# Kernel optimization log

Hardware: AMD Instinct MI355X
Metric: run time of the kernel (lower is better)

The kernel has to match this reference:

```python
import jax, jax.numpy as jnp
import numpy as np

NL = 4      # num_layers
DM = 1024   # hidden_size (d_model)
DI = 2048   # d_inner = expand * d_model
DS = 16     # d_state
DC = 4      # d_conv
DTR = 64    # dt_rank = ceil(d_model/16)
IN = 256    # input_size
OUT = 128   # output_size
B = 4096    # batch


def setup_inputs() -> dict:
    key = jax.random.key(0)
    ks = jax.random.split(key, 10)
    s = 0.02
    d = {}
    d['x'] = jax.random.normal(ks[0], (B, IN), dtype=jnp.float32)
    d['inp_w'] = jax.random.normal(ks[1], (DM, IN), dtype=jnp.float32) * s
    d['inp_b'] = jnp.zeros((DM,), jnp.float32)
    d['in_proj_w'] = jax.random.normal(ks[2], (NL, 2 * DI, DM), dtype=jnp.float32) * s
    d['conv_w'] = jax.random.normal(ks[3], (NL, DI, DC), dtype=jnp.float32) * s
    d['conv_b'] = jnp.zeros((NL, DI), jnp.float32)
    d['xproj_w'] = jax.random.normal(ks[4], (NL, DTR + 2 * DS, DI), dtype=jnp.float32) * s
    d['dt_w'] = jax.random.normal(ks[5], (NL, DI, DTR), dtype=jnp.float32) * s
    dt_init = jax.random.uniform(ks[6], (NL, DI), minval=1e-3, maxval=1e-1)
    d['dt_b'] = jnp.log(jnp.expm1(dt_init))  # softplus^-1 of target dt
    d['A_log'] = jnp.log(jnp.broadcast_to(jnp.arange(1, DS + 1, dtype=jnp.float32), (NL, DI, DS)))
    d['D_param'] = jnp.ones((NL, DI), jnp.float32)
    d['out_w'] = jax.random.normal(ks[7], (NL, DM, DI), dtype=jnp.float32) * s
    d['ln_g'] = jnp.ones((NL, DM), jnp.float32)
    d['ln_b'] = jnp.zeros((NL, DM), jnp.float32)
    d['outp_w'] = jax.random.normal(ks[8], (OUT, DM), dtype=jnp.float32) * s
    d['outp_b'] = jnp.zeros((OUT,), jnp.float32)
    return d


def _silu(x):
    return x * jax.nn.sigmoid(x)


def _layer_norm(x, g, b, eps=1e-5):
    mu = jnp.mean(x, axis=-1, keepdims=True)
    var = jnp.mean(jnp.square(x - mu), axis=-1, keepdims=True)
    return (x - mu) * jax.lax.rsqrt(var + eps) * g + b


def _mamba_block(x, in_w, cw, cb, xp_w, dtw, dtb, A_log, Dp, ow):
    # x: [B, L, DM]
    Bn, Ls, _ = x.shape
    xz = jnp.einsum('bld,ed->ble', x, in_w)              # [B,L,2*DI]
    xc, z = jnp.split(xz, 2, axis=-1)
    # causal depthwise conv1d (kernel DC, groups=DI)
    xpad = jnp.pad(xc, ((0, 0), (DC - 1, 0), (0, 0)))
    conv = cb + sum(xpad[:, k:k + Ls, :] * cw[:, k] for k in range(DC))
    xc = _silu(conv)
    x_dbl = jnp.einsum('bld,ed->ble', xc, xp_w)           # [B,L,DTR+2*DS]
    dt, Bm, Cm = jnp.split(x_dbl, [DTR, DTR + DS], axis=-1)
    dt = jax.nn.softplus(jnp.einsum('blr,dr->bld', dt, dtw) + dtb)  # [B,L,DI]
    A = -jnp.exp(A_log)                                   # [DI,DS]

    def step(h, inp):
        dt_t, B_t, C_t, x_t = inp                         # [B,DI],[B,DS],[B,DS],[B,DI]
        h = jnp.exp(dt_t[..., None] * A) * h + dt_t[..., None] * B_t[:, None, :] * x_t[..., None]
        y = jnp.einsum('bdn,bn->bd', h, C_t)
        return h, y

    h0 = jnp.zeros((Bn, DI, DS), dtype=x.dtype)
    xs = (jnp.moveaxis(dt, 1, 0), jnp.moveaxis(Bm, 1, 0), jnp.moveaxis(Cm, 1, 0), jnp.moveaxis(xc, 1, 0))
    _, ys = jax.lax.scan(step, h0, xs)
    y = jnp.moveaxis(ys, 0, 1) + Dp * xc                  # [B,L,DI]
    y = y * _silu(z)
    return jnp.einsum('bld,md->blm', y, ow)               # [B,L,DM]


def reference(x, inp_w, inp_b, in_proj_w, conv_w, conv_b, xproj_w, dt_w, dt_b,
              A_log, D_param, out_w, ln_g, ln_b, outp_w, outp_b):
    h = x[:, None, :]                                     # unsqueeze(1): [B,1,IN]
    h = jnp.einsum('bli,di->bld', h, inp_w) + inp_b       # input_proj
    for i in range(NL):
        res = h
        y = _mamba_block(h, in_proj_w[i], conv_w[i], conv_b[i], xproj_w[i],
                         dt_w[i], dt_b[i], A_log[i], D_param[i], out_w[i])
        y = _layer_norm(y, ln_g[i], ln_b[i])
        h = res + y                                       # dropout is identity in eval
    h = h[:, 0, :]                                        # squeeze(1)
    return jnp.einsum('bd,od->bo', h, outp_w) + outp_b
```

## Files before the change

kernel.cpp:

```cpp
#include <hip/hip_runtime.h>
#include <hip/hip_bf16.h>
#include <hip/hip_fp16.h>

#define NL 4
#define DM 1024
#define DI 2048
#define DS_N 16
#define DC 4
#define DTR 64
#define IN_DIM 256
#define OUT_DIM 128
#define BATCH 4096

typedef _Float16 half8 __attribute__((ext_vector_type(8)));
typedef _Float16 half4 __attribute__((ext_vector_type(4)));
typedef float floatx4 __attribute__((ext_vector_type(4)));

#define E_X      0L
#define E_INPW   (E_X + (long)BATCH * IN_DIM)
#define E_INPROJ (E_INPW + (long)DM * IN_DIM)
#define E_XPROJ  (E_INPROJ + (long)NL * 2 * DI * DM)
#define E_DTW    (E_XPROJ + (long)NL * (DTR + 2 * DS_N) * DI)
#define E_OUTW   (E_DTW + (long)NL * DI * DTR)
#define E_OUTPW  (E_OUTW + (long)NL * DM * DI)
#define E_TOT    (E_OUTPW + (long)OUT_DIM * DM)

__device__ __forceinline__ float silu_f(float x) {
    return x / (1.0f + __expf(-x));
}

__device__ __forceinline__ void gload_lds16(const _Float16* g, const _Float16* l) {
    __builtin_amdgcn_global_load_lds(
        (const __attribute__((address_space(1))) void*)(uintptr_t)g,
        (__attribute__((address_space(3))) void*)(uintptr_t)l,
        16, 0, 0);
}

__global__ __launch_bounds__(256) void cvt_k(
    const float* __restrict__ x, const float* __restrict__ inp_w,
    const float* __restrict__ in_proj_w, const float* __restrict__ xproj_w,
    const float* __restrict__ dt_w, const float* __restrict__ out_w,
    const float* __restrict__ outp_w, _Float16* __restrict__ dst)
{
    long i = ((long)blockIdx.x * 256 + threadIdx.x) * 8;
    const float* s;
    if      (i < E_INPW)   s = x         + (i - E_X);
    else if (i < E_INPROJ) s = inp_w     + (i - E_INPW);
    else if (i < E_XPROJ)  s = in_proj_w + (i - E_INPROJ);
    else if (i < E_DTW)    s = xproj_w   + (i - E_XPROJ);
    else if (i < E_OUTW)   s = dt_w      + (i - E_DTW);
    else if (i < E_OUTPW)  s = out_w     + (i - E_OUTW);
    else                   s = outp_w    + (i - E_OUTPW);
    float4 a = *(const float4*)s;
    float4 b = *(const float4*)(s + 4);
    half8 h;
    h[0]=(_Float16)a.x; h[1]=(_Float16)a.y; h[2]=(_Float16)a.z; h[3]=(_Float16)a.w;
    h[4]=(_Float16)b.x; h[5]=(_Float16)b.y; h[6]=(_Float16)b.z; h[7]=(_Float16)b.w;
    *(half8*)(dst + i) = h;
}

struct EpiP {
    float* o32;
    _Float16* o16;
    _Float16* o16b;
    const float* bias;
    const float* cw;
    const float* cb;
    const float* dtb;
    const float* Dp;
    const _Float16* xc;
    const _Float16* zs;
};

template<int EPI>
__global__ __launch_bounds__(256) void gemm_k(
    const _Float16* __restrict__ A, const _Float16* __restrict__ W,
    int N, int K, int lda, int kChunk, EpiP ep)
{
    __shared__ __align__(16) char smem[32768];
    const int tid  = threadIdx.x;
    const int lane = tid & 63;
    const int wave = tid >> 6;
    const int wm = (wave >> 1) * 64;
    const int wn = (wave & 1) * 64;
    const int lr = lane & 15;
    const int lq = lane >> 4;
    const long tm = (long)blockIdx.y * 128;
    const int  tn = blockIdx.x * 128;

    const int p0 = wave * 128 + lane;
    const int r0 = p0 >> 2, c0 = ((p0 & 3) - ((r0 >> 1) & 3)) & 3;
    const int p1 = p0 + 64;
    const int r1 = p1 >> 2, c1 = ((p1 & 3) - ((r1 >> 1) & 3)) & 3;

    const int kBeg = blockIdx.z * kChunk;
    const _Float16* a0 = A + (tm + r0) * (long)lda + kBeg + c0 * 8;
    const _Float16* a1 = A + (tm + r1) * (long)lda + kBeg + c1 * 8;
    const _Float16* w0 = W + (long)min(tn + r0, N - 1) * K + kBeg + c0 * 8;
    const _Float16* w1 = W + (long)min(tn + r1, N - 1) * K + kBeg + c1 * 8;

    floatx4 acc[4][4];
#pragma unroll
    for (int i = 0; i < 4; i++)
#pragma unroll
        for (int j = 0; j < 4; j++) acc[i][j] = (floatx4)0.0f;

    const int iters = kChunk / 32;
    auto stage = [&](int b) {
        _Float16* As = (_Float16*)(smem + b * 16384);
        _Float16* Bs = (_Float16*)(smem + b * 16384 + 8192);
        gload_lds16(a0, &As[wave * 1024]);
        gload_lds16(a1, &As[wave * 1024 + 512]);
        gload_lds16(w0, &Bs[wave * 1024]);
        gload_lds16(w1, &Bs[wave * 1024 + 512]);
        a0 += 32; a1 += 32; w0 += 32; w1 += 32;
    };

    stage(0);
    for (int it = 0; it < iters; it++) {
        __syncthreads();
        if (it + 1 < iters) stage((it + 1) & 1);
        const _Float16* As = (const _Float16*)(smem + (it & 1) * 16384);
        const _Float16* Bs = As + 4096;

        half8 af[4], bf[4];
#pragma unroll
        for (int i = 0; i < 4; i++) {
            int row = wm + i * 16 + lr;
            int slot = row * 4 + ((lq + (row >> 1)) & 3);
            af[i] = *(const half8*)&As[slot * 8];
        }
#pragma unroll
        for (int j = 0; j < 4; j++) {
            int row = wn + j * 16 + lr;
            int slot = row * 4 + ((lq + (row >> 1)) & 3);
            bf[j] = *(const half8*)&Bs[slot * 8];
        }
#pragma unroll
        for (int i = 0; i < 4; i++)
#pragma unroll
            for (int j = 0; j < 4; j++)
                acc[i][j] = __builtin_amdgcn_mfma_f32_16x16x32_f16(af[i], bf[j], acc[i][j], 0, 0, 0);
    }
    __syncthreads();

    if constexpr (EPI != 5) {
        const int rsub = lane >> 3;
        const int cch  = lane & 7;
        const int cb0  = tn + wn;
        const int n0   = cb0 + cch * 8;
        const long g0  = tm + wm;

        float bv[8], cwv[8], dtbv[8], dpv[8];
        if constexpr (EPI == 0) {
            float4 q0 = *(const float4*)&ep.bias[n0];
            float4 q1 = *(const float4*)&ep.bias[n0 + 4];
            bv[0]=q0.x; bv[1]=q0.y; bv[2]=q0.z; bv[3]=q0.w;
            bv[4]=q1.x; bv[5]=q1.y; bv[6]=q1.z; bv[7]=q1.w;
        }
        if constexpr (EPI == 1) {
            if (cb0 < DI) {
#pragma unroll
                for (int k = 0; k < 8; k++) cwv[k] = ep.cw[(n0 + k) * DC + 3];
                float4 q0 = *(const float4*)&ep.cb[n0];
                float4 q1 = *(const float4*)&ep.cb[n0 + 4];
                bv[0]=q0.x; bv[1]=q0.y; bv[2]=q0.z; bv[3]=q0.w;
                bv[4]=q1.x; bv[5]=q1.y; bv[6]=q1.z; bv[7]=q1.w;
            }
        }
        float bcv;
        if constexpr (EPI == 3) {
            float4 q0 = *(const float4*)&ep.dtb[n0];
            float4 q1 = *(const float4*)&ep.dtb[n0 + 4];
            dtbv[0]=q0.x; dtbv[1]=q0.y; dtbv[2]=q0.z; dtbv[3]=q0.w;
            dtbv[4]=q1.x; dtbv[5]=q1.y; dtbv[6]=q1.z; dtbv[7]=q1.w;
            float4 p0v = *(const float4*)&ep.Dp[n0];
            float4 p1v = *(const float4*)&ep.Dp[n0 + 4];
            dpv[0]=p0v.x; dpv[1]=p0v.y; dpv[2]=p0v.z; dpv[3]=p0v.w;
            dpv[4]=p1v.x; dpv[5]=p1v.y; dpv[6]=p1v.z; dpv[7]=p1v.w;
            const half8* pp = (const half8*)(A + (g0 + lane) * 96 + DTR);
            half8 b0 = pp[0], b1 = pp[1], c0v = pp[2], c1v = pp[3];
            float s = 0.0f;
#pragma unroll
            for (int k = 0; k < 8; k++)
                s += (float)b0[k] * (float)c0v[k] + (float)b1[k] * (float)c1v[k];
            bcv = s;
        }

        _Float16* slab = (_Float16*)(smem + wave * 4608);
#pragma unroll
        for (int rr = 0; rr < 2; rr++) {
#pragma unroll
            for (int i2 = 0; i2 < 2; i2++)
#pragma unroll
                for (int j = 0; j < 4; j++)
#pragma unroll
                    for (int p = 0; p < 4; p++)
                        slab[(i2 * 16 + lq * 4 + p) * 72 + j * 16 + lr] =
                            (_Float16)acc[rr * 2 + i2][j][p];

#pragma unroll
            for (int r = 0; r < 4; r++) {
                int rloc = rr * 32 + r * 8 + rsub;
                long g = g0 + rloc;
                half8 hv = *(const half8*)&slab[(r * 8 + rsub) * 72 + cch * 8];
                if constexpr (EPI == 0) {
                    float4 f0, f1; half8 o;
#pragma unroll
                    for (int k = 0; k < 4; k++) {
                        float v = (float)hv[k] + bv[k];
                        (&f0.x)[k] = v; o[k] = (_Float16)v;
                    }
#pragma unroll
                    for (int k = 0; k < 4; k++) {
                        float v = (float)hv[k + 4] + bv[k + 4];
                        (&f1.x)[k] = v; o[k + 4] = (_Float16)v;
                    }
                    *(float4*)&ep.o32[g * DM + n0]     = f0;
                    *(float4*)&ep.o32[g * DM + n0 + 4] = f1;
                    *(half8*)&ep.o16[g * DM + n0] = o;
                } else if constexpr (EPI == 1) {
                    half8 o;
                    if (cb0 < DI) {
#pragma unroll
                        for (int k = 0; k < 8; k++) {
                            float s = (float)hv[k] * cwv[k] + bv[k];
                            o[k] = (_Float16)silu_f(s);
                        }
                        *(half8*)&ep.o16[g * DI + n0] = o;
                    } else {
#pragma unroll
                        for (int k = 0; k < 8; k++) o[k] = (_Float16)silu_f((float)hv[k]);
                        *(half8*)&ep.o16b[g * DI + (n0 - DI)] = o;
                    }
                } else if constexpr (EPI == 3) {
                    float bc = __shfl(bcv, rloc, 64);
                    half8 xcv = *(const half8*)&ep.xc[g * DI + n0];
                    half8 zsv = *(const half8*)&ep.zs[g * DI + n0];
                    half8 o;
#pragma unroll
                    for (int k = 0; k < 8; k++) {
                        float dtv = (float)hv[k] + dtbv[k];
                        dtv = (dtv > 20.0f) ? dtv : log1pf(__expf(dtv));
                        float y = (float)xcv[k] * (dtv * bc + dpv[k]) * (float)zsv[k];
                        o[k] = (_Float16)y;
                    }
                    *(half8*)&ep.o16[g * DI + n0] = o;
                } else if constexpr (EPI == 4) {
                    *(half8*)&ep.o16[((long)blockIdx.z * BATCH + g) * DM + n0] = hv;
                } else {
                    if (n0 < 96)
                        *(half8*)&ep.o16[((long)blockIdx.z * BATCH + g) * 96 + n0] = hv;
                }
            }
            if (rr == 0) __builtin_amdgcn_s_waitcnt(0);
        }
    } else {
#pragma unroll
        for (int i = 0; i < 4; i++) {
#pragma unroll
            for (int p = 0; p < 4; p++) {
                long m = tm + wm + i * 16 + lq * 4 + p;
#pragma unroll
                for (int j = 0; j < 4; j++) {
                    int n = tn + wn + j * 16 + lr;
                    if (n >= N) continue;
                    ep.o32[m * OUT_DIM + n] = acc[i][j][p] + ep.bias[n];
                }
            }
        }
    }
}

__global__ __launch_bounds__(256) void xred_k(
    const _Float16* __restrict__ part, _Float16* __restrict__ xdbl)
{
    long i = ((long)blockIdx.x * 256 + threadIdx.x) * 4;
    float s0 = 0.f, s1 = 0.f, s2 = 0.f, s3 = 0.f;
#pragma unroll
    for (int z = 0; z < 8; z++) {
        half4 v = *(const half4*)&part[(long)z * BATCH * 96 + i];
        s0 += (float)v[0]; s1 += (float)v[1]; s2 += (float)v[2]; s3 += (float)v[3];
    }
    half4 h;
    h[0] = (_Float16)s0; h[1] = (_Float16)s1; h[2] = (_Float16)s2; h[3] = (_Float16)s3;
    *(half4*)&xdbl[i] = h;
}

__global__ __launch_bounds__(256) void ln_k(
    const _Float16* __restrict__ xin, const float* __restrict__ g, const float* __restrict__ b,
    float* __restrict__ h32, _Float16* __restrict__ h16)
{
    long row = blockIdx.x;
    const _Float16* x0 = xin + row * DM;
    const _Float16* x1 = xin + ((long)BATCH + row) * DM;
    int t = threadIdx.x;
    float v[4];
    float s = 0.0f, ss = 0.0f;
#pragma unroll
    for (int i = 0; i < 4; i++) {
        int c = t + i * 256;
        v[i] = (float)x0[c] + (float)x1[c];
        s += v[i];
        ss += v[i] * v[i];
    }
#pragma unroll
    for (int o = 32; o > 0; o >>= 1) {
        s  += __shfl_down(s, o, 64);
        ss += __shfl_down(ss, o, 64);
    }
    __shared__ float rs[4], rss[4];
    int wv = t >> 6, ln = t & 63;
    if (ln == 0) { rs[wv] = s; rss[wv] = ss; }
    __syncthreads();
    if (t == 0) {
        float S  = rs[0] + rs[1] + rs[2] + rs[3];
        float SS = rss[0] + rss[1] + rss[2] + rss[3];
        float mu = S / (float)DM;
        float var = SS / (float)DM - mu * mu;
        rs[0]  = mu;
        rss[0] = rsqrtf(var + 1e-5f);
    }
    __syncthreads();
    float mu = rs[0], rstd = rss[0];
#pragma unroll
    for (int i = 0; i < 4; i++) {
        int c = t + i * 256;
        float hv = h32[row * DM + c] + (v[i] - mu) * rstd * g[c] + b[c];
        h32[row * DM + c] = hv;
        h16[row * DM + c] = (_Float16)hv;
    }
}

extern "C" void kernel_launch(void* const* d_in, const int* in_sizes, int n_in,
                              void* d_out, int out_size, void* d_ws, size_t ws_size,
                              hipStream_t stream) {
    const float* x         = (const float*)d_in[0];
    const float* inp_w     = (const float*)d_in[1];
    const float* inp_b     = (const float*)d_in[2];
    const float* in_proj_w = (const float*)d_in[3];
    const float* conv_w    = (const float*)d_in[4];
    const float* conv_b    = (const float*)d_in[5];
    const float* xproj_w   = (const float*)d_in[6];
    const float* dt_w      = (const float*)d_in[7];
    const float* dt_b      = (const float*)d_in[8];
    const float* D_param   = (const float*)d_in[10];
    const float* out_w     = (const float*)d_in[11];
    const float* ln_g      = (const float*)d_in[12];
    const float* ln_b      = (const float*)d_in[13];
    const float* outp_w    = (const float*)d_in[14];
    const float* outp_b    = (const float*)d_in[15];

    char* ws = (char*)d_ws;
    _Float16* wf    = (_Float16*)ws;
    float*    h32   = (float*)   (ws + (56u  << 20));
    _Float16* h16   = (_Float16*)(ws + (72u  << 20));
    _Float16* xc16  = (_Float16*)(ws + (80u  << 20));
    _Float16* zs16  = (_Float16*)(ws + (96u  << 20));
    _Float16* lnin16= (_Float16*)(ws + (96u  << 20));
    _Float16* xdbl  = (_Float16*)(ws + (112u << 20));
    _Float16* xpart = (_Float16*)(ws + (114u << 20));

    dim3 blk(256);
    EpiP ep;

    cvt_k<<<dim3((unsigned)(E_TOT / (256 * 8))), blk, 0, stream>>>(
        x, inp_w, in_proj_w, xproj_w, dt_w, out_w, outp_w, wf);

    ep = EpiP{}; ep.bias = inp_b; ep.o32 = h32; ep.o16 = h16;
    gemm_k<0><<<dim3(DM / 128, BATCH / 128, 1), blk, 0, stream>>>(
        wf + E_X, wf + E_INPW, DM, IN_DIM, IN_DIM, IN_DIM, ep);

    for (int l = 0; l < NL; l++) {
        ep = EpiP{}; ep.o16 = xc16; ep.o16b = zs16;
        ep.cw = conv_w + (size_t)l * DI * DC; ep.cb = conv_b + (size_t)l * DI;
        gemm_k<1><<<dim3(2 * DI / 128, BATCH / 128, 1), blk, 0, stream>>>(
            h16, wf + E_INPROJ + (size_t)l * 2 * DI * DM, 2 * DI, DM, DM, DM, ep);

        ep = EpiP{}; ep.o16 = xpart;
        gemm_k<6><<<dim3(1, BATCH / 128, 8), blk, 0, stream>>>(
            xc16, wf + E_XPROJ + (size_t)l * (DTR + 2 * DS_N) * DI,
            DTR + 2 * DS_N, DI, DI, DI / 8, ep);

        xred_k<<<dim3(BATCH * 96 / 4 / 256), blk, 0, stream>>>(xpart, xdbl);

        ep = EpiP{}; ep.o16 = xc16;
        ep.dtb = dt_b + (size_t)l * DI; ep.Dp = D_param + (size_t)l * DI;
        ep.xc = xc16; ep.zs = zs16;
        gemm_k<3><<<dim3(DI / 128, BATCH / 128, 1), blk, 0, stream>>>(
            xdbl, wf + E_DTW + (size_t)l * DI * DTR, DI, DTR, 96, DTR, ep);

        ep = EpiP{}; ep.o16 = lnin16;
        gemm_k<4><<<dim3(DM / 128, BATCH / 128, 2), blk, 0, stream>>>(
            xc16, wf + E_OUTW + (size_t)l * DM * DI, DM, DI, DI, DI / 2, ep);

        ln_k<<<dim3(BATCH), blk, 0, stream>>>(
            lnin16, ln_g + (size_t)l * DM, ln_b + (size_t)l * DM, h32, h16);
    }

    ep = EpiP{}; ep.bias = outp_b; ep.o32 = (float*)d_out;
    gemm_k<5><<<dim3(1, BATCH / 128, 1), blk, 0, stream>>>(
        h16, wf + E_OUTPW, OUT_DIM, DM, DM, DM, ep);
}
```

Baseline: 745.5 us.

## Remap GEMM tiles per XCD and raise split-K for x_proj and out_proj

Gives GEMM blocks with gridDim.z==1 a new tile index, so that blocks assigned round-robin to the same XCD (id & 7) cover a contiguous band of M rows and share the A operand in that XCD's L2. The split-K factor doubles for the x_proj GEMM (8 to 16) and the out_proj GEMM (2 to 4), which launches more blocks and shortens each K loop. The extra partial buffers are summed in xred_k and ln_k. In exchange the partial sums cost more memory traffic, and the second out_proj buffer reuses the xpart region.

```diff
diff --git a/kernel.cpp b/kernel.cpp
--- a/kernel.cpp
+++ b/kernel.cpp
@@ -85,8 +85,18 @@
     const int wn = (wave & 1) * 64;
     const int lr = lane & 15;
     const int lq = lane >> 4;
-    const long tm = (long)blockIdx.y * 128;
-    const int  tn = blockIdx.x * 128;
+
+    int tmb = blockIdx.y, tnb = blockIdx.x;
+    if (gridDim.z == 1 && gridDim.x >= 8 && (gridDim.y & 7) == 0) {
+        int id = blockIdx.y * gridDim.x + blockIdx.x;
+        int r = id & 7;
+        int lid = id >> 3;
+        int rowsPerR = gridDim.y >> 3;
+        tmb = r * rowsPerR + lid / gridDim.x;
+        tnb = lid % gridDim.x;
+    }
+    const long tm = (long)tmb * 128;
+    const int  tn = tnb * 128;
 
     const int p0 = wave * 128 + lane;
     const int r0 = p0 >> 2, c0 = ((p0 & 3) - ((r0 >> 1) & 3)) & 3;
@@ -247,7 +257,8 @@
                     }
                     *(half8*)&ep.o16[g * DI + n0] = o;
                 } else if constexpr (EPI == 4) {
-                    *(half8*)&ep.o16[((long)blockIdx.z * BATCH + g) * DM + n0] = hv;
+                    _Float16* dst = (blockIdx.z < 2) ? ep.o16 : ep.o16b;
+                    *(half8*)&dst[(((long)(blockIdx.z & 1)) * BATCH + g) * DM + n0] = hv;
                 } else {
                     if (n0 < 96)
                         *(half8*)&ep.o16[((long)blockIdx.z * BATCH + g) * 96 + n0] = hv;
@@ -278,7 +289,7 @@
     long i = ((long)blockIdx.x * 256 + threadIdx.x) * 4;
     float s0 = 0.f, s1 = 0.f, s2 = 0.f, s3 = 0.f;
 #pragma unroll
-    for (int z = 0; z < 8; z++) {
+    for (int z = 0; z < 16; z++) {
         half4 v = *(const half4*)&part[(long)z * BATCH * 96 + i];
         s0 += (float)v[0]; s1 += (float)v[1]; s2 += (float)v[2]; s3 += (float)v[3];
     }
@@ -288,19 +299,22 @@
 }
 
 __global__ __launch_bounds__(256) void ln_k(
-    const _Float16* __restrict__ xin, const float* __restrict__ g, const float* __restrict__ b,
+    const _Float16* __restrict__ xinA, const _Float16* __restrict__ xinB,
+    const float* __restrict__ g, const float* __restrict__ b,
     float* __restrict__ h32, _Float16* __restrict__ h16)
 {
     long row = blockIdx.x;
-    const _Float16* x0 = xin + row * DM;
-    const _Float16* x1 = xin + ((long)BATCH + row) * DM;
+    const _Float16* xa0 = xinA + row * DM;
+    const _Float16* xa1 = xinA + ((long)BATCH + row) * DM;
+    const _Float16* xb0 = xinB + row * DM;
+    const _Float16* xb1 = xinB + ((long)BATCH + row) * DM;
     int t = threadIdx.x;
     float v[4];
     float s = 0.0f, ss = 0.0f;
 #pragma unroll
     for (int i = 0; i < 4; i++) {
         int c = t + i * 256;
-        v[i] = (float)x0[c] + (float)x1[c];
+        v[i] = (float)xa0[c] + (float)xa1[c] + (float)xb0[c] + (float)xb1[c];
         s += v[i];
         ss += v[i] * v[i];
     }
@@ -357,9 +371,10 @@
     _Float16* h16   = (_Float16*)(ws + (72u  << 20));
     _Float16* xc16  = (_Float16*)(ws + (80u  << 20));
     _Float16* zs16  = (_Float16*)(ws + (96u  << 20));
-    _Float16* lnin16= (_Float16*)(ws + (96u  << 20));
+    _Float16* lninA = (_Float16*)(ws + (96u  << 20));
     _Float16* xdbl  = (_Float16*)(ws + (112u << 20));
     _Float16* xpart = (_Float16*)(ws + (114u << 20));
+    _Float16* lninB = (_Float16*)(ws + (114u << 20));
 
     dim3 blk(256);
     EpiP ep;
@@ -378,9 +393,9 @@
             h16, wf + E_INPROJ + (size_t)l * 2 * DI * DM, 2 * DI, DM, DM, DM, ep);
 
         ep = EpiP{}; ep.o16 = xpart;
-        gemm_k<6><<<dim3(1, BATCH / 128, 8), blk, 0, stream>>>(
+        gemm_k<6><<<dim3(1, BATCH / 128, 16), blk, 0, stream>>>(
             xc16, wf + E_XPROJ + (size_t)l * (DTR + 2 * DS_N) * DI,
-            DTR + 2 * DS_N, DI, DI, DI / 8, ep);
+            DTR + 2 * DS_N, DI, DI, DI / 16, ep);
 
         xred_k<<<dim3(BATCH * 96 / 4 / 256), blk, 0, stream>>>(xpart, xdbl);
 
@@ -390,12 +405,12 @@
         gemm_k<3><<<dim3(DI / 128, BATCH / 128, 1), blk, 0, stream>>>(
             xdbl, wf + E_DTW + (size_t)l * DI * DTR, DI, DTR, 96, DTR, ep);
 
-        ep = EpiP{}; ep.o16 = lnin16;
-        gemm_k<4><<<dim3(DM / 128, BATCH / 128, 2), blk, 0, stream>>>(
-            xc16, wf + E_OUTW + (size_t)l * DM * DI, DM, DI, DI, DI / 2, ep);
+        ep = EpiP{}; ep.o16 = lninA; ep.o16b = lninB;
+        gemm_k<4><<<dim3(DM / 128, BATCH / 128, 4), blk, 0, stream>>>(
+            xc16, wf + E_OUTW + (size_t)l * DM * DI, DM, DI, DI, DI / 4, ep);
 
         ln_k<<<dim3(BATCH), blk, 0, stream>>>(
-            lnin16, ln_g + (size_t)l * DM, ln_b + (size_t)l * DM, h32, h16);
+            lninA, lninB, ln_g + (size_t)l * DM, ln_b + (size_t)l * DM, h32, h16);
     }
 
     ep = EpiP{}; ep.bias = outp_b; ep.o32 = (float*)d_out;
```

Result: slower. 787.6 us (+5.7%).
